# Performance work log

Hardware: AMD Instinct MI355X
Metric: run time of the kernel (lower is better)

The kernel has to match this reference:

```python
import jax, jax.numpy as jnp
import numpy as np

N_NODES = 50000
N_EDGES = 800000
DIM = 128
NUM_LAYERS = 4


def setup_inputs() -> dict:
    key = jax.random.key(0)
    ks = jax.random.split(key, 7)
    x = jax.random.normal(ks[0], (N_NODES, DIM), dtype=jnp.float32)
    edge_index = jax.random.randint(ks[1], (2, N_EDGES), 0, N_NODES, dtype=jnp.int64)
    batch = jnp.zeros((N_NODES,), dtype=jnp.int64)
    scale = 1.0 / np.sqrt(DIM)
    W1 = jax.random.normal(ks[2], (NUM_LAYERS, DIM, DIM), dtype=jnp.float32) * scale
    b1 = jax.random.normal(ks[3], (NUM_LAYERS, DIM), dtype=jnp.float32) * scale
    W2 = jax.random.normal(ks[4], (NUM_LAYERS, DIM, DIM), dtype=jnp.float32) * scale
    b2 = jax.random.normal(ks[5], (NUM_LAYERS, DIM), dtype=jnp.float32) * scale
    return {"x": x, "edge_index": edge_index, "batch": batch,
            "W1": W1, "b1": b1, "W2": W2, "b2": b2}


def reference(x, edge_index, batch, W1, b1, W2, b2):
    # Stacked GINConv (eps=0): h = MLP(x + sum_{j->i} x_j)
    src, dst = edge_index[0], edge_index[1]
    for l in range(NUM_LAYERS):
        agg = x + jax.ops.segment_sum(x[src], dst, num_segments=N_NODES)
        h = jax.nn.relu(agg @ W1[l] + b1[l])
        x = h @ W2[l] + b2[l]
    return x
```

## Files before the change

### kernel.cpp

```cpp
#include <hip/hip_runtime.h>
#include <hip/hip_bf16.h>
#include <cstdint>

#define N_NODES 50000
#define N_EDGES 800000
#define DIM     128
#define NLAYERS 4

#define SCAN_BLK 256
#define NB ((N_NODES + SCAN_BLK - 1) / SCAN_BLK)


__global__ __launch_bounds__(256) void zero_kernel(int* __restrict__ p, int n) {
    int i = blockIdx.x * blockDim.x + threadIdx.x;
    if (i < n) p[i] = 0;
}

__global__ __launch_bounds__(256) void count_kernel(const int* __restrict__ dst,
                                                    int* __restrict__ cnt) {
    int e = blockIdx.x * blockDim.x + threadIdx.x;
    if (e < N_EDGES) atomicAdd(&cnt[dst[e]], 1);
}

__global__ __launch_bounds__(SCAN_BLK) void scanA(const int* __restrict__ cnt,
                                                  int* __restrict__ off,
                                                  int* __restrict__ bsum) {
    __shared__ int s[SCAN_BLK];
    const int t = threadIdx.x;
    const int i = blockIdx.x * SCAN_BLK + t;
    int v = (i < N_NODES) ? cnt[i] : 0;
    s[t] = v;
    __syncthreads();
    for (int d = 1; d < SCAN_BLK; d <<= 1) {
        int add = (t >= d) ? s[t - d] : 0;
        __syncthreads();
        s[t] += add;
        __syncthreads();
    }
    if (i < N_NODES) off[i] = s[t] - v;
    if (t == SCAN_BLK - 1) bsum[blockIdx.x] = s[t];
}

__global__ __launch_bounds__(SCAN_BLK) void scanB(int* __restrict__ bsum) {
    __shared__ int s[SCAN_BLK];
    const int t = threadIdx.x;
    int v = (t < NB) ? bsum[t] : 0;
    s[t] = v;
    __syncthreads();
    for (int d = 1; d < SCAN_BLK; d <<= 1) {
        int add = (t >= d) ? s[t - d] : 0;
        __syncthreads();
        s[t] += add;
        __syncthreads();
    }
    if (t < NB) bsum[t] = s[t] - v;
}

__global__ __launch_bounds__(SCAN_BLK) void scanC(int* __restrict__ off,
                                                  const int* __restrict__ bsum,
                                                  int* __restrict__ cur) {
    const int i = blockIdx.x * SCAN_BLK + threadIdx.x;
    if (i < N_NODES) {
        int o = off[i] + bsum[blockIdx.x];
        off[i] = o;
        cur[i] = o;
    }
    if (i == 0) off[N_NODES] = N_EDGES;
}

__global__ __launch_bounds__(256) void scatter_kernel(const int* __restrict__ src,
                                                      const int* __restrict__ dst,
                                                      int* __restrict__ cur,
                                                      int* __restrict__ csr) {
    int e = blockIdx.x * blockDim.x + threadIdx.x;
    if (e < N_EDGES) {
        int d = dst[e];
        int pos = atomicAdd(&cur[d], 1);
        csr[pos] = src[e];
    }
}


#define RT 32
#define LDW 132
#define MAXE 1024

__global__ __launch_bounds__(256) void gin_layer(
    const float* __restrict__ xin, const int* __restrict__ off,
    const int* __restrict__ csr,
    const float* __restrict__ W1, const float* __restrict__ b1,
    const float* __restrict__ W2, const float* __restrict__ b2,
    float* __restrict__ xout)
{
    __shared__ float sA[RT][LDW];
    __shared__ int   sIdx[MAXE];
    __shared__ int   sOff[RT + 1];
    const int tid  = threadIdx.x;
    const int base = blockIdx.x * RT;
    const int rtop = min(RT, N_NODES - base);

    if (tid <= rtop) sOff[tid] = off[base + tid];
    __syncthreads();

    const int e0 = sOff[0];
    const int nE = sOff[rtop] - e0;
    const bool staged = (nE <= MAXE);
    if (staged) {
        for (int i = tid; i < nE; i += 256) sIdx[i] = csr[e0 + i];
    }
    __syncthreads();

    {
        const int c = tid & 31;
        const int g = tid >> 5;
        const float4* xin4 = reinterpret_cast<const float4*>(xin);
        #pragma unroll
        for (int it = 0; it < 4; ++it) {
            const int rr = g + it * 8;
            if (rr < rtop) {
                const int node = base + rr;
                float4 a = xin4[node * 32 + c];
                const int k0 = sOff[rr] - e0, k1 = sOff[rr + 1] - e0;
                int k = k0;
                if (staged) {
                    for (; k + 8 <= k1; k += 8) {
                        int id[8];
                        #pragma unroll
                        for (int j = 0; j < 8; ++j) id[j] = sIdx[k + j];
                        float4 v0 = xin4[id[0] * 32 + c];
                        float4 v1 = xin4[id[1] * 32 + c];
                        float4 v2 = xin4[id[2] * 32 + c];
                        float4 v3 = xin4[id[3] * 32 + c];
                        float4 v4 = xin4[id[4] * 32 + c];
                        float4 v5 = xin4[id[5] * 32 + c];
                        float4 v6 = xin4[id[6] * 32 + c];
                        float4 v7 = xin4[id[7] * 32 + c];
                        a.x += ((v0.x + v1.x) + (v2.x + v3.x)) + ((v4.x + v5.x) + (v6.x + v7.x));
                        a.y += ((v0.y + v1.y) + (v2.y + v3.y)) + ((v4.y + v5.y) + (v6.y + v7.y));
                        a.z += ((v0.z + v1.z) + (v2.z + v3.z)) + ((v4.z + v5.z) + (v6.z + v7.z));
                        a.w += ((v0.w + v1.w) + (v2.w + v3.w)) + ((v4.w + v5.w) + (v6.w + v7.w));
                    }
                    for (; k < k1; ++k) {
                        float4 v = xin4[sIdx[k] * 32 + c];
                        a.x += v.x; a.y += v.y; a.z += v.z; a.w += v.w;
                    }
                } else {
                    for (; k < k1; ++k) {
                        float4 v = xin4[csr[e0 + k] * 32 + c];
                        a.x += v.x; a.y += v.y; a.z += v.z; a.w += v.w;
                    }
                }
                *reinterpret_cast<float4*>(&sA[rr][c * 4]) = a;
            }
        }
    }
    __syncthreads();

    const int tc = tid & 31;
    const int tr = tid >> 5;

    float acc[4][4] = {};
    {
        const float4* Wv = reinterpret_cast<const float4*>(W1);
        #pragma unroll 4
        for (int k4 = 0; k4 < DIM / 4; ++k4) {
            float4 w[4];
            #pragma unroll
            for (int j = 0; j < 4; ++j) w[j] = Wv[(k4 * 4 + j) * 32 + tc];
            #pragma unroll
            for (int i = 0; i < 4; ++i) {
                const float4 a = *reinterpret_cast<const float4*>(&sA[tr * 4 + i][k4 * 4]);
                acc[i][0] += a.x * w[0].x + a.y * w[1].x + a.z * w[2].x + a.w * w[3].x;
                acc[i][1] += a.x * w[0].y + a.y * w[1].y + a.z * w[2].y + a.w * w[3].y;
                acc[i][2] += a.x * w[0].z + a.y * w[1].z + a.z * w[2].z + a.w * w[3].z;
                acc[i][3] += a.x * w[0].w + a.y * w[1].w + a.z * w[2].w + a.w * w[3].w;
            }
        }
        const float4 b = reinterpret_cast<const float4*>(b1)[tc];
        #pragma unroll
        for (int i = 0; i < 4; ++i) {
            acc[i][0] = fmaxf(acc[i][0] + b.x, 0.f);
            acc[i][1] = fmaxf(acc[i][1] + b.y, 0.f);
            acc[i][2] = fmaxf(acc[i][2] + b.z, 0.f);
            acc[i][3] = fmaxf(acc[i][3] + b.w, 0.f);
        }
    }
    __syncthreads();

    #pragma unroll
    for (int i = 0; i < 4; ++i) {
        float4 h;
        h.x = acc[i][0]; h.y = acc[i][1]; h.z = acc[i][2]; h.w = acc[i][3];
        *reinterpret_cast<float4*>(&sA[tr * 4 + i][tc * 4]) = h;
    }
    __syncthreads();

    {
        float acc2[4][4] = {};
        const float4* Wv = reinterpret_cast<const float4*>(W2);
        #pragma unroll 4
        for (int k4 = 0; k4 < DIM / 4; ++k4) {
            float4 w[4];
            #pragma unroll
            for (int j = 0; j < 4; ++j) w[j] = Wv[(k4 * 4 + j) * 32 + tc];
            #pragma unroll
            for (int i = 0; i < 4; ++i) {
                const float4 a = *reinterpret_cast<const float4*>(&sA[tr * 4 + i][k4 * 4]);
                acc2[i][0] += a.x * w[0].x + a.y * w[1].x + a.z * w[2].x + a.w * w[3].x;
                acc2[i][1] += a.x * w[0].y + a.y * w[1].y + a.z * w[2].y + a.w * w[3].y;
                acc2[i][2] += a.x * w[0].z + a.y * w[1].z + a.z * w[2].z + a.w * w[3].z;
                acc2[i][3] += a.x * w[0].w + a.y * w[1].w + a.z * w[2].w + a.w * w[3].w;
            }
        }
        const float4 b = reinterpret_cast<const float4*>(b2)[tc];
        #pragma unroll
        for (int i = 0; i < 4; ++i) {
            const int node = base + tr * 4 + i;
            if (node < N_NODES) {
                float4 o;
                o.x = acc2[i][0] + b.x;
                o.y = acc2[i][1] + b.y;
                o.z = acc2[i][2] + b.z;
                o.w = acc2[i][3] + b.w;
                reinterpret_cast<float4*>(xout + node * DIM)[tc] = o;
            }
        }
    }
}


extern "C" void kernel_launch(void* const* d_in, const int* in_sizes, int n_in,
                              void* d_out, int out_size, void* d_ws, size_t ws_size,
                              hipStream_t stream) {
    const float* x  = (const float*)d_in[0];
    const int*   ei = (const int*)d_in[1];
    const float* W1 = (const float*)d_in[3];
    const float* b1 = (const float*)d_in[4];
    const float* W2 = (const float*)d_in[5];
    const float* b2 = (const float*)d_in[6];
    float* out = (float*)d_out;

    const int* src = ei;
    const int* dst = ei + N_EDGES;

    float* bufA = (float*)d_ws;
    int*   cnt  = (int*)(bufA + (size_t)N_NODES * DIM);
    int*   offs = cnt + N_NODES;
    int*   cur  = offs + N_NODES + 1;
    int*   bsum = cur + N_NODES;
    int*   csr  = bsum + 256;

    zero_kernel<<<NB, 256, 0, stream>>>(cnt, N_NODES);
    count_kernel<<<(N_EDGES + 255) / 256, 256, 0, stream>>>(dst, cnt);
    scanA<<<NB, SCAN_BLK, 0, stream>>>(cnt, offs, bsum);
    scanB<<<1, SCAN_BLK, 0, stream>>>(bsum);
    scanC<<<NB, SCAN_BLK, 0, stream>>>(offs, bsum, cur);
    scatter_kernel<<<(N_EDGES + 255) / 256, 256, 0, stream>>>(src, dst, cur, csr);

    const int nblk = (N_NODES + RT - 1) / RT;
    gin_layer<<<nblk, 256, 0, stream>>>(x,    offs, csr, W1 + 0 * DIM * DIM, b1 + 0 * DIM,
                                        W2 + 0 * DIM * DIM, b2 + 0 * DIM, bufA);
    gin_layer<<<nblk, 256, 0, stream>>>(bufA, offs, csr, W1 + 1 * DIM * DIM, b1 + 1 * DIM,
                                        W2 + 1 * DIM * DIM, b2 + 1 * DIM, out);
    gin_layer<<<nblk, 256, 0, stream>>>(out,  offs, csr, W1 + 2 * DIM * DIM, b1 + 2 * DIM,
                                        W2 + 2 * DIM * DIM, b2 + 2 * DIM, bufA);
    gin_layer<<<nblk, 256, 0, stream>>>(bufA, offs, csr, W1 + 3 * DIM * DIM, b1 + 3 * DIM,
                                        W2 + 3 * DIM * DIM, b2 + 3 * DIM, out);
}
```

Before: 764.0 us.

## Build CSR with source-bucketed two-pass scatter for locality-ordered neighbor lists

Replaces the single atomic scatter into the destination CSR with a two-pass build. Edges are first bucketed by source into a CSC, then each source thread walks its edges and appends itself into the destination CSR. Each destination's neighbor list therefore tends to come out roughly sorted by source, which should improve cache locality of the x[src] gathers in the four layer kernels. The cost is an extra count, scan and scatter pass, more workspace, and a serial per-thread loop in order_kernel that can hit contended atomics and load imbalance.

```diff
diff --git a/kernel.cpp b/kernel.cpp
--- a/kernel.cpp
+++ b/kernel.cpp
@@ -16,10 +16,10 @@
     if (i < n) p[i] = 0;
 }
 
-__global__ __launch_bounds__(256) void count_kernel(const int* __restrict__ dst,
+__global__ __launch_bounds__(256) void count_kernel(const int* __restrict__ key,
                                                     int* __restrict__ cnt) {
     int e = blockIdx.x * blockDim.x + threadIdx.x;
-    if (e < N_EDGES) atomicAdd(&cnt[dst[e]], 1);
+    if (e < N_EDGES) atomicAdd(&cnt[key[e]], 1);
 }
 
 __global__ __launch_bounds__(SCAN_BLK) void scanA(const int* __restrict__ cnt,
@@ -68,15 +68,30 @@
     if (i == 0) off[N_NODES] = N_EDGES;
 }
 
-__global__ __launch_bounds__(256) void scatter_kernel(const int* __restrict__ src,
-                                                      const int* __restrict__ dst,
-                                                      int* __restrict__ cur,
-                                                      int* __restrict__ csr) {
+__global__ __launch_bounds__(256) void bucket_src_kernel(const int* __restrict__ src,
+                                                         const int* __restrict__ dst,
+                                                         int* __restrict__ cur2,
+                                                         int* __restrict__ csc_dst) {
     int e = blockIdx.x * blockDim.x + threadIdx.x;
     if (e < N_EDGES) {
-        int d = dst[e];
-        int pos = atomicAdd(&cur[d], 1);
-        csr[pos] = src[e];
+        int s = src[e];
+        int pos = atomicAdd(&cur2[s], 1);
+        csc_dst[pos] = dst[e];
+    }
+}
+
+__global__ __launch_bounds__(256) void order_kernel(const int* __restrict__ off2,
+                                                    const int* __restrict__ csc_dst,
+                                                    int* __restrict__ cur,
+                                                    int* __restrict__ csr) {
+    int s = blockIdx.x * blockDim.x + threadIdx.x;
+    if (s < N_NODES) {
+        const int p0 = off2[s], p1 = off2[s + 1];
+        for (int p = p0; p < p1; ++p) {
+            int d = csc_dst[p];
+            int pos = atomicAdd(&cur[d], 1);
+            csr[pos] = s;
+        }
     }
 }
 
@@ -243,19 +258,29 @@
     const int* src = ei;
     const int* dst = ei + N_EDGES;
 
-    float* bufA = (float*)d_ws;
-    int*   cnt  = (int*)(bufA + (size_t)N_NODES * DIM);
-    int*   offs = cnt + N_NODES;
-    int*   cur  = offs + N_NODES + 1;
-    int*   bsum = cur + N_NODES;
-    int*   csr  = bsum + 256;
-
-    zero_kernel<<<NB, 256, 0, stream>>>(cnt, N_NODES);
+    float* bufA    = (float*)d_ws;
+    int*   cnt     = (int*)(bufA + (size_t)N_NODES * DIM);
+    int*   cnt2    = cnt + N_NODES;
+    int*   offs    = cnt2 + N_NODES;
+    int*   off2    = offs + N_NODES + 1;
+    int*   cur     = off2 + N_NODES + 1;
+    int*   cur2    = cur + N_NODES;
+    int*   bsum    = cur2 + N_NODES;
+    int*   bsum2   = bsum + 256;
+    int*   csr     = bsum2 + 256;
+    int*   csc_dst = csr + N_EDGES;
+
+    zero_kernel<<<(2 * N_NODES + 255) / 256, 256, 0, stream>>>(cnt, 2 * N_NODES);
     count_kernel<<<(N_EDGES + 255) / 256, 256, 0, stream>>>(dst, cnt);
+    count_kernel<<<(N_EDGES + 255) / 256, 256, 0, stream>>>(src, cnt2);
     scanA<<<NB, SCAN_BLK, 0, stream>>>(cnt, offs, bsum);
     scanB<<<1, SCAN_BLK, 0, stream>>>(bsum);
     scanC<<<NB, SCAN_BLK, 0, stream>>>(offs, bsum, cur);
-    scatter_kernel<<<(N_EDGES + 255) / 256, 256, 0, stream>>>(src, dst, cur, csr);
+    scanA<<<NB, SCAN_BLK, 0, stream>>>(cnt2, off2, bsum2);
+    scanB<<<1, SCAN_BLK, 0, stream>>>(bsum2);
+    scanC<<<NB, SCAN_BLK, 0, stream>>>(off2, bsum2, cur2);
+    bucket_src_kernel<<<(N_EDGES + 255) / 256, 256, 0, stream>>>(src, dst, cur2, csc_dst);
+    order_kernel<<<NB, 256, 0, stream>>>(off2, csc_dst, cur, csr);
 
     const int nblk = (N_NODES + RT - 1) / RT;
     gin_layer<<<nblk, 256, 0, stream>>>(x,    offs, csr, W1 + 0 * DIM * DIM, b1 + 0 * DIM,
```

Result: slower. 818.2 us (+7.1%).
